# Performance work log

Measured on AMD Instinct MI355X. Metric: run time of the kernel, lower is better.

The kernel has to match this reference:

```python
import jax, jax.numpy as jnp
import numpy as np

EPS = 1e-5  # BatchNorm2d default eps


def conv1x1_bn(x, w, g, b, m, v):
    # 1x1 conv (no bias) + inference BatchNorm folded to scale/shift
    y = jnp.einsum('bchw,oc->bohw', x, w)
    s = g / jnp.sqrt(v + EPS)
    return y * s[None, :, None, None] + (b - m * s)[None, :, None, None]


def setup_inputs() -> dict:
    key = jax.random.key(0)
    ks = jax.random.split(key, 18)
    B, C, H, W = 4, 256, 64, 64
    KD, NH = 16, 8
    DH = KD * NH
    f = jax.random.normal
    u = jax.random.uniform
    return {
        'x': f(ks[0], (B, C, H, W), jnp.float32),
        'key_v_input_reduction': f(ks[1], (1,), jnp.float32),
        'w_qk': f(ks[2], (KD, C), jnp.float32) * 0.05,
        'g_qk': u(ks[3], (KD,), jnp.float32, 0.5, 1.5),
        'b_qk': f(ks[4], (KD,), jnp.float32) * 0.05,
        'm_qk': f(ks[5], (KD,), jnp.float32) * 0.05,
        'v_qk': u(ks[6], (KD,), jnp.float32, 0.5, 1.5),
        'w_v': f(ks[7], (DH, C), jnp.float32) * 0.05,
        'g_v': u(ks[8], (DH,), jnp.float32, 0.5, 1.5),
        'b_v': f(ks[9], (DH,), jnp.float32) * 0.05,
        'm_v': f(ks[10], (DH,), jnp.float32) * 0.05,
        'v_v': u(ks[11], (DH,), jnp.float32, 0.5, 1.5),
        'w_p': f(ks[12], (C, DH), jnp.float32) * 0.05,
        'g_p': u(ks[13], (C,), jnp.float32, 0.5, 1.5),
        'b_p': f(ks[14], (C,), jnp.float32) * 0.05,
        'm_p': f(ks[15], (C,), jnp.float32) * 0.05,
        'v_p': u(ks[16], (C,), jnp.float32, 0.5, 1.5),
    }


def reference(x, key_v_input_reduction, w_qk, g_qk, b_qk, m_qk, v_qk,
              w_v, g_v, b_v, m_v, v_v, w_p, g_p, b_p, m_p, v_p):
    B, C, H, W = x.shape
    N = H * W
    kd = w_qk.shape[0]
    dh = w_v.shape[0]
    nh = dh // kd
    # shared single KV head: qq == kk (share_kv=True, one_kv_head=True)
    qk = conv1x1_bn(x, w_qk, g_qk, b_qk, m_qk, v_qk).reshape(B, 1, kd, N)
    qq = jnp.swapaxes(qk, -1, -2)                      # [B,1,N,kd]
    attn = jax.nn.softmax(jnp.matmul(qq, qk), axis=-1)  # [B,1,N,N]
    vv = conv1x1_bn(x, w_v, g_v, b_v, m_v, v_v).reshape(B, nh, kd, N)
    vv = jnp.swapaxes(vv, -1, -2)                      # [B,nh,N,kd]
    xx = jnp.matmul(attn, vv)                          # broadcast head dim -> [B,nh,N,kd]
    xx = jnp.swapaxes(xx, -1, -2).reshape(B, dh, H, W)
    out = conv1x1_bn(jax.nn.relu(xx), w_p, g_p, b_p, m_p, v_p)
    return out
```

## Files before the change

### kernel.cpp

```cpp
#include <hip/hip_runtime.h>
#include <cstdint>
#include <cstddef>


typedef __attribute__((ext_vector_type(4)))  float f32x4;
typedef __attribute__((ext_vector_type(16))) float f32x16;
typedef __attribute__((ext_vector_type(8)))  _Float16 half8;
typedef __attribute__((ext_vector_type(8)))  unsigned short ushort8;
typedef __attribute__((ext_vector_type(2)))  unsigned u32x2;
typedef __attribute__((ext_vector_type(4)))  unsigned u32x4;

#define N_SP 4096
#define CIN  256
#define KDIM 16
#define DHV  128

__device__ __forceinline__ unsigned short f2h(float f) {
    _Float16 h = (_Float16)f;
    return __builtin_bit_cast(unsigned short, h);
}
__device__ __forceinline__ float h2f(unsigned short u) {
    return (float)__builtin_bit_cast(_Float16, u);
}
__device__ __forceinline__ unsigned pk2(float a, float b) {
    return (unsigned)f2h(a) | ((unsigned)f2h(b) << 16);
}
__device__ __forceinline__ unsigned shfl32u(unsigned v, int src) {
    return (unsigned)__shfl((int)v, src, 64);
}
__device__ __forceinline__ f32x4 mfma16(ushort8 a, ushort8 b, f32x4 c) {
    return __builtin_amdgcn_mfma_f32_16x16x32_f16(
        __builtin_bit_cast(half8, a), __builtin_bit_cast(half8, b), c, 0, 0, 0);
}
__device__ __forceinline__ f32x16 mfma32(half8 a, half8 b, f32x16 c) {
    return __builtin_amdgcn_mfma_f32_32x32x16_f16(a, b, c, 0, 0, 0);
}

__global__ __launch_bounds__(256) void fold_weights(
    const float* __restrict__ w_qk, const float* __restrict__ g_qk,
    const float* __restrict__ b_qk, const float* __restrict__ m_qk,
    const float* __restrict__ v_qk,
    const float* __restrict__ w_v, const float* __restrict__ g_v,
    const float* __restrict__ b_v, const float* __restrict__ m_v,
    const float* __restrict__ v_v,
    const float* __restrict__ w_p, const float* __restrict__ g_p,
    const float* __restrict__ b_p, const float* __restrict__ m_p,
    const float* __restrict__ v_p,
    unsigned short* __restrict__ wf1, float* __restrict__ shift1,
    unsigned short* __restrict__ wpf, float* __restrict__ shiftp)
{
    const float SQL2E = 1.2011224087864498f;
    int row = blockIdx.x;
    int t   = threadIdx.x;
    if (row < 144) {
        float s, sh; const float* src;
        if (row < KDIM) {
            s  = g_qk[row] * rsqrtf(v_qk[row] + 1e-5f);
            sh = b_qk[row] - m_qk[row] * s;
            s *= SQL2E; sh *= SQL2E;
            src = w_qk + row * CIN;
        } else {
            int o = row - KDIM;
            s  = g_v[o] * rsqrtf(v_v[o] + 1e-5f);
            sh = b_v[o] - m_v[o] * s;
            src = w_v + o * CIN;
        }
        wf1[row * CIN + t] = f2h(src[t] * s);
        if (t == 0) shift1[row] = sh;
    } else {
        int o = row - 144;
        float s = g_p[o] * rsqrtf(v_p[o] + 1e-5f);
        if (t < DHV) wpf[o * DHV + t] = f2h(w_p[o * DHV + t] * s);
        if (t == 0) shiftp[o] = b_p[o] - m_p[o] * s;
    }
}

__global__ __launch_bounds__(512) void proj_qkv(
    const float* __restrict__ x,
    const unsigned short* __restrict__ wf1, const float* __restrict__ shift1,
    unsigned short* __restrict__ qkT, unsigned short* __restrict__ Vt)
{
    const int b  = blockIdx.y;
    const int n0 = blockIdx.x * 64;
    const int tid  = threadIdx.x;
    const int w    = tid >> 6;
    const int half = w >> 2;
    const int wq   = w & 3;
    const int lane = tid & 63;
    const int lg   = lane >> 4;
    const int lr   = lane & 15;
    const int n    = n0 + wq * 16 + lr;

    const float* xb = x + (size_t)b * CIN * N_SP;

    if (half == 0) {
        f32x4 acc[5];
#pragma unroll
        for (int i = 0; i < 5; ++i) acc[i] = (f32x4){0.f, 0.f, 0.f, 0.f};
        for (int ks = 0; ks < 8; ++ks) {
            const int cbase = ks * 32 + lg * 8;
            ushort8 bx;
#pragma unroll
            for (int j = 0; j < 8; ++j)
                bx[j] = f2h(xb[(size_t)(cbase + j) * N_SP + n]);
#pragma unroll
            for (int i = 0; i < 5; ++i) {
                ushort8 a = *(const ushort8*)(wf1 + (i * 16 + lr) * CIN + cbase);
                acc[i] = mfma16(a, bx, acc[i]);
            }
        }
#pragma unroll
        for (int i = 0; i < 5; ++i)
#pragma unroll
            for (int r = 0; r < 4; ++r) {
                int o = i * 16 + lg * 4 + r;
                float val = acc[i][r] + shift1[o];
                unsigned short hv = f2h(val);
                if (o < KDIM) qkT[((size_t)b * N_SP + n) * 16 + o] = hv;
                else          Vt[((size_t)b * DHV + (o - KDIM)) * N_SP + n] = hv;
            }
    } else {
        f32x4 acc[4];
#pragma unroll
        for (int i = 0; i < 4; ++i) acc[i] = (f32x4){0.f, 0.f, 0.f, 0.f};
        for (int ks = 0; ks < 8; ++ks) {
            const int cbase = ks * 32 + lg * 8;
            ushort8 bx;
#pragma unroll
            for (int j = 0; j < 8; ++j)
                bx[j] = f2h(xb[(size_t)(cbase + j) * N_SP + n]);
#pragma unroll
            for (int i = 0; i < 4; ++i) {
                ushort8 a = *(const ushort8*)(wf1 + ((i + 5) * 16 + lr) * CIN + cbase);
                acc[i] = mfma16(a, bx, acc[i]);
            }
        }
#pragma unroll
        for (int i = 0; i < 4; ++i)
#pragma unroll
            for (int r = 0; r < 4; ++r) {
                int o = (i + 5) * 16 + lg * 4 + r;
                float val = acc[i][r] + shift1[o];
                Vt[((size_t)b * DHV + (o - KDIM)) * N_SP + n] = f2h(val);
            }
    }
}

__device__ __forceinline__ void stage_v(
    const unsigned short* __restrict__ vt_b,
    unsigned short* v_l, int k0, int p, int lane)
{
#pragma unroll
    for (int s = 0; s < 8; ++s) {
        const int vi = p * 8 + s;
        const int d  = vi * 8 + (lane >> 3);
        const int c8 = (lane & 7) ^ ((lane >> 3) & 7);
        const unsigned short* src = vt_b + (size_t)d * N_SP + k0 + c8 * 8;
        __builtin_amdgcn_global_load_lds(
            (const __attribute__((address_space(1))) void*)src,
            (__attribute__((address_space(3))) void*)(v_l + vi * 512),
            16, 0, 0);
    }
}

__device__ __forceinline__ half8 ldv(const unsigned short* vl, int nb, int kc,
                                     int la31, int hi)
{
    const int d = nb * 32 + la31;
    const ushort8 v = *(const ushort8*)
        (vl + d * 64 + (((kc * 2 + hi) ^ (d & 7)) << 3));
    return __builtin_bit_cast(half8, v);
}

__device__ __forceinline__ half8 ldk(const unsigned short* qk_b, int krow,
                                     int la31, int hi)
{
    return __builtin_bit_cast(half8,
        *(const ushort8*)(qk_b + (size_t)(krow + la31) * 16 + hi * 8));
}

__global__ __launch_bounds__(512, 2) void attn_kernel(
    const unsigned short* __restrict__ qkT,
    const unsigned short* __restrict__ Vt,
    const unsigned short* __restrict__ wpf,
    const float* __restrict__ shiftp,
    float* __restrict__ out)
{
    const int b  = blockIdx.y;
    const int q0 = blockIdx.x * 64;
    const int tid  = threadIdx.x;
    const int ws   = tid >> 6;
    const int strm = ws >> 1;
    const int p    = ws & 1;
    const int lane = tid & 63;
    const int la31 = lane & 31;
    const int hi   = lane >> 5;

    const unsigned short* qk_b = qkT + (size_t)b * N_SP * 16;
    const unsigned short* vt_b = Vt  + (size_t)b * DHV * N_SP;
    const int kbase = strm * (N_SP / 4);
    const int qrow  = q0 + p * 32;

    const half8 aq = __builtin_bit_cast(half8,
        *(const ushort8*)(qk_b + (size_t)(qrow + la31) * 16 + hi * 8));

    f32x16 acc0, acc1, acc2, acc3, z16;
#pragma unroll
    for (int i = 0; i < 16; ++i) { z16[i] = 0.f; }
    acc0 = z16; acc1 = z16; acc2 = z16; acc3 = z16;
    float m_r = -__builtin_inff();
    float l_r = 0.f;

    __shared__ __align__(16) unsigned short v_lds[4][2][128 * 64];
    __shared__ float lmbuf[4][64][2];

    stage_v(vt_b, &v_lds[strm][0][0], kbase, p, lane);
    half8 kf0n = ldk(qk_b, kbase, la31, hi);
    half8 kf1n = ldk(qk_b, kbase + 32, la31, hi);

    for (int t = 0; t < 16; ++t) {
        const int cur = t & 1;
        __syncthreads();
        if (t < 15)
            stage_v(vt_b, &v_lds[strm][cur ^ 1][0], kbase + (t + 1) * 64,
                    p, lane);
        const half8 kf0 = kf0n;
        const half8 kf1 = kf1n;
        if (t < 15) {
            kf0n = ldk(qk_b, kbase + (t + 1) * 64, la31, hi);
            kf1n = ldk(qk_b, kbase + (t + 1) * 64 + 32, la31, hi);
        }
        const unsigned short* vl = &v_lds[strm][cur][0];

        f32x16 s0 = mfma32(kf0, aq, z16);
        f32x16 s1 = mfma32(kf1, aq, z16);

        float mpair[8];
#pragma unroll
        for (int i = 0; i < 8; ++i)
            mpair[i] = fmaxf(fmaxf(s0[i], s0[i + 8]), fmaxf(s1[i], s1[i + 8]));
        float mx = fmaxf(fmaxf(fmaxf(mpair[0], mpair[1]), fmaxf(mpair[2], mpair[3])),
                         fmaxf(fmaxf(mpair[4], mpair[5]), fmaxf(mpair[6], mpair[7])));
        mx = fmaxf(mx, __shfl(mx, lane ^ 32));

        if (!__all(mx <= m_r + 11.54f)) {
            float mnew = fmaxf(m_r, mx);
            float sc = exp2f(m_r - mnew);
            l_r *= sc;
#pragma unroll
            for (int i = 0; i < 16; ++i) {
                acc0[i] *= sc; acc1[i] *= sc; acc2[i] *= sc; acc3[i] *= sc;
            }
            m_r = mnew;
        }
#pragma unroll
        for (int i = 0; i < 16; ++i) s0[i] = exp2f(s0[i] - m_r);
#pragma unroll
        for (int i = 0; i < 16; ++i) s1[i] = exp2f(s1[i] - m_r);
        float rpair[8];
#pragma unroll
        for (int i = 0; i < 8; ++i)
            rpair[i] = (s0[i] + s0[i + 8]) + (s1[i] + s1[i + 8]);
        l_r += ((rpair[0] + rpair[1]) + (rpair[2] + rpair[3]))
             + ((rpair[4] + rpair[5]) + (rpair[6] + rpair[7]));

#define PV_CHUNK(SV, B0, KC)                                               \
        {                                                                  \
            unsigned a0 = pk2(SV[B0 + 0], SV[B0 + 1]);                     \
            unsigned a1 = pk2(SV[B0 + 2], SV[B0 + 3]);                     \
            unsigned a2 = pk2(SV[B0 + 4], SV[B0 + 5]);                     \
            unsigned a3 = pk2(SV[B0 + 6], SV[B0 + 7]);                     \
            unsigned p0 = shfl32u(a0, lane ^ 32);                          \
            unsigned p1 = shfl32u(a1, lane ^ 32);                          \
            unsigned p2 = shfl32u(a2, lane ^ 32);                          \
            unsigned p3 = shfl32u(a3, lane ^ 32);                          \
            u32x4 pw;                                                      \
            pw.x = hi ? p2 : a0;                                           \
            pw.y = hi ? p3 : a1;                                           \
            pw.z = hi ? a2 : p0;                                           \
            pw.w = hi ? a3 : p1;                                           \
            half8 pb = __builtin_bit_cast(half8, pw);                      \
            acc0 = mfma32(ldv(vl, 0, KC, la31, hi), pb, acc0);             \
            acc1 = mfma32(ldv(vl, 1, KC, la31, hi), pb, acc1);             \
            acc2 = mfma32(ldv(vl, 2, KC, la31, hi), pb, acc2);             \
            acc3 = mfma32(ldv(vl, 3, KC, la31, hi), pb, acc3);             \
        }
        PV_CHUNK(s0, 0, 0)
        PV_CHUNK(s0, 8, 1)
        PV_CHUNK(s1, 0, 2)
        PV_CHUNK(s1, 8, 3)
#undef PV_CHUNK
    }

    l_r = l_r + __shfl(l_r, lane ^ 32);

    __syncthreads();

    unsigned short* Opart = &v_lds[0][0][0];
    const int qib = p * 32 + la31;
    if (hi == 0) {
        lmbuf[strm][qib][0] = m_r;
        lmbuf[strm][qib][1] = l_r;
    }
    {
        const float invl = 1.0f / l_r;
        const size_t qoff = ((size_t)strm * 64 + qib) * 128;
#define PUB(ACC, NB)                                                       \
        {                                                                  \
            _Pragma("unroll")                                              \
            for (int rq = 0; rq < 4; ++rq) {                               \
                float v0 = ACC[rq * 4 + 0] * invl;                         \
                float v1 = ACC[rq * 4 + 1] * invl;                         \
                float v2 = ACC[rq * 4 + 2] * invl;                         \
                float v3 = ACC[rq * 4 + 3] * invl;                         \
                u32x2 wv; wv.x = pk2(v0, v1); wv.y = pk2(v2, v3);          \
                *(u32x2*)(Opart + qoff + NB * 32 + rq * 8 + 4 * hi) = wv;  \
            }                                                              \
        }
        PUB(acc0, 0) PUB(acc1, 1) PUB(acc2, 2) PUB(acc3, 3)
#undef PUB
    }
    __syncthreads();

    unsigned short* olds = &v_lds[2][0][0];
    {
        const int q    = tid >> 3;
        const int dseg = (tid & 7) * 16;
        const float m0 = lmbuf[0][q][0], l0 = lmbuf[0][q][1];
        const float m1 = lmbuf[1][q][0], l1 = lmbuf[1][q][1];
        const float m2 = lmbuf[2][q][0], l2 = lmbuf[2][q][1];
        const float m3 = lmbuf[3][q][0], l3 = lmbuf[3][q][1];
        const float M = fmaxf(fmaxf(m0, m1), fmaxf(m2, m3));
        float w0 = l0 * exp2f(m0 - M);
        float w1 = l1 * exp2f(m1 - M);
        float w2 = l2 * exp2f(m2 - M);
        float w3 = l3 * exp2f(m3 - M);
        const float inv = 1.0f / (w0 + w1 + w2 + w3);
        w0 *= inv; w1 *= inv; w2 *= inv; w3 *= inv;

        const ushort8 A0 = *(const ushort8*)(Opart + (0 * 64 + q) * 128 + dseg);
        const ushort8 A1 = *(const ushort8*)(Opart + (1 * 64 + q) * 128 + dseg);
        const ushort8 A2 = *(const ushort8*)(Opart + (2 * 64 + q) * 128 + dseg);
        const ushort8 A3 = *(const ushort8*)(Opart + (3 * 64 + q) * 128 + dseg);
        const ushort8 B0 = *(const ushort8*)(Opart + (0 * 64 + q) * 128 + dseg + 8);
        const ushort8 B1 = *(const ushort8*)(Opart + (1 * 64 + q) * 128 + dseg + 8);
        const ushort8 B2 = *(const ushort8*)(Opart + (2 * 64 + q) * 128 + dseg + 8);
        const ushort8 B3 = *(const ushort8*)(Opart + (3 * 64 + q) * 128 + dseg + 8);

        ushort8 o0, o1;
#pragma unroll
        for (int i = 0; i < 8; ++i) {
            float va = w0 * h2f(A0[i]) + w1 * h2f(A1[i])
                     + w2 * h2f(A2[i]) + w3 * h2f(A3[i]);
            float vb = w0 * h2f(B0[i]) + w1 * h2f(B1[i])
                     + w2 * h2f(B2[i]) + w3 * h2f(B3[i]);
            o0[i] = f2h(fmaxf(va, 0.f));
            o1[i] = f2h(fmaxf(vb, 0.f));
        }
        *(ushort8*)(olds + q * 136 + dseg)     = o0;
        *(ushort8*)(olds + q * 136 + dseg + 8) = o1;
    }
    __syncthreads();

    {
        const int lr16 = lane & 15;
        const int lg16 = lane >> 4;
        const int ob   = ws * 32;

        f32x4 pacc[2][4];
#pragma unroll
        for (int i = 0; i < 2; ++i)
#pragma unroll
            for (int j = 0; j < 4; ++j) pacc[i][j] = (f32x4){0.f, 0.f, 0.f, 0.f};

        for (int ks = 0; ks < 4; ++ks) {
            ushort8 a0 = *(const ushort8*)
                (wpf + (size_t)(ob + lr16) * DHV + ks * 32 + lg16 * 8);
            ushort8 a1 = *(const ushort8*)
                (wpf + (size_t)(ob + 16 + lr16) * DHV + ks * 32 + lg16 * 8);
#pragma unroll
            for (int qt = 0; qt < 4; ++qt) {
                ushort8 bfr = *(const ushort8*)
                    (olds + (qt * 16 + lr16) * 136 + ks * 32 + lg16 * 8);
                pacc[0][qt] = mfma16(a0, bfr, pacc[0][qt]);
                pacc[1][qt] = mfma16(a1, bfr, pacc[1][qt]);
            }
        }

#pragma unroll
        for (int t2 = 0; t2 < 2; ++t2)
#pragma unroll
            for (int qt = 0; qt < 4; ++qt)
#pragma unroll
                for (int r = 0; r < 4; ++r) {
                    int o = ob + t2 * 16 + lg16 * 4 + r;
                    out[((size_t)b * CIN + o) * N_SP + q0 + qt * 16 + lr16]
                        = pacc[t2][qt][r] + shiftp[o];
                }
    }
}

extern "C" void kernel_launch(void* const* d_in, const int* in_sizes, int n_in,
                              void* d_out, int out_size, void* d_ws, size_t ws_size,
                              hipStream_t stream)
{
    const float* x    = (const float*)d_in[0];
    const float* w_qk = (const float*)d_in[2];
    const float* g_qk = (const float*)d_in[3];
    const float* b_qk = (const float*)d_in[4];
    const float* m_qk = (const float*)d_in[5];
    const float* v_qk = (const float*)d_in[6];
    const float* w_v  = (const float*)d_in[7];
    const float* g_v  = (const float*)d_in[8];
    const float* b_v  = (const float*)d_in[9];
    const float* m_v  = (const float*)d_in[10];
    const float* v_v  = (const float*)d_in[11];
    const float* w_p  = (const float*)d_in[12];
    const float* g_p  = (const float*)d_in[13];
    const float* b_p  = (const float*)d_in[14];
    const float* m_p  = (const float*)d_in[15];
    const float* v_p  = (const float*)d_in[16];

    char* ws = (char*)d_ws;
    unsigned short* qkT = (unsigned short*)(ws);
    unsigned short* Vt  = (unsigned short*)(ws + (1u << 20));
    unsigned short* wf1 = (unsigned short*)(ws + (9u << 20));
    float* shift1       = (float*)(ws + (9u << 20) + 80 * 1024);
    unsigned short* wpf = (unsigned short*)(ws + (9u << 20) + 84 * 1024);
    float* shiftp       = (float*)(ws + (9u << 20) + 148 * 1024);

    fold_weights<<<400, 256, 0, stream>>>(
        w_qk, g_qk, b_qk, m_qk, v_qk,
        w_v, g_v, b_v, m_v, v_v,
        w_p, g_p, b_p, m_p, v_p,
        wf1, shift1, wpf, shiftp);

    proj_qkv<<<dim3(64, 4), 512, 0, stream>>>(x, wf1, shift1, qkT, Vt);

    attn_kernel<<<dim3(64, 4), 512, 0, stream>>>(
        qkT, Vt, wpf, shiftp, (float*)d_out);
}
```

Before: 69.94 us.

## Split attention keys across eight wave-pair streams with 1024-thread blocks

The attention kernel now runs 1024 threads per block, so the key dimension is split into 8 streams instead of 4. Each stream handles 512 keys in 32-key tiles with a narrower swizzled LDS V buffer, and the final merge combines 8 partial outputs. The projection epilogue gives each wave 16 output channels instead of 32. The aim is more waves per CU to hide latency in the key loop. The cost is a larger cross-stream merge, more barriers per tile, and heavier register pressure under the new launch bounds.

```diff
diff --git a/kernel.cpp b/kernel.cpp
--- a/kernel.cpp
+++ b/kernel.cpp
@@ -151,11 +151,12 @@
     unsigned short* v_l, int k0, int p, int lane)
 {
 #pragma unroll
-    for (int s = 0; s < 8; ++s) {
-        const int vi = p * 8 + s;
-        const int d  = vi * 8 + (lane >> 3);
-        const int c8 = (lane & 7) ^ ((lane >> 3) & 7);
-        const unsigned short* src = vt_b + (size_t)d * N_SP + k0 + c8 * 8;
+    for (int s = 0; s < 4; ++s) {
+        const int vi   = p * 4 + s;
+        const int dloc = lane >> 2;
+        const int d    = vi * 16 + dloc;
+        const int c4   = (lane & 3) ^ (dloc & 3);
+        const unsigned short* src = vt_b + (size_t)d * N_SP + k0 + c4 * 8;
         __builtin_amdgcn_global_load_lds(
             (const __attribute__((address_space(1))) void*)src,
             (__attribute__((address_space(3))) void*)(v_l + vi * 512),
@@ -168,7 +169,7 @@
 {
     const int d = nb * 32 + la31;
     const ushort8 v = *(const ushort8*)
-        (vl + d * 64 + (((kc * 2 + hi) ^ (d & 7)) << 3));
+        (vl + d * 32 + (((kc * 2 + hi) ^ (d & 3)) << 3));
     return __builtin_bit_cast(half8, v);
 }
 
@@ -179,7 +180,7 @@
         *(const ushort8*)(qk_b + (size_t)(krow + la31) * 16 + hi * 8));
 }
 
-__global__ __launch_bounds__(512, 2) void attn_kernel(
+__global__ __launch_bounds__(1024, 4) void attn_kernel(
     const unsigned short* __restrict__ qkT,
     const unsigned short* __restrict__ Vt,
     const unsigned short* __restrict__ wpf,
@@ -198,7 +199,7 @@
 
     const unsigned short* qk_b = qkT + (size_t)b * N_SP * 16;
     const unsigned short* vt_b = Vt  + (size_t)b * DHV * N_SP;
-    const int kbase = strm * (N_SP / 4);
+    const int kbase = strm * (N_SP / 8);
     const int qrow  = q0 + p * 32;
 
     const half8 aq = __builtin_bit_cast(half8,
@@ -211,34 +212,28 @@
     float m_r = -__builtin_inff();
     float l_r = 0.f;
 
-    __shared__ __align__(16) unsigned short v_lds[4][2][128 * 64];
-    __shared__ float lmbuf[4][64][2];
+    __shared__ __align__(16) unsigned short v_lds[8][2][128 * 32];
+    __shared__ float lmbuf[8][64][2];
 
     stage_v(vt_b, &v_lds[strm][0][0], kbase, p, lane);
     half8 kf0n = ldk(qk_b, kbase, la31, hi);
-    half8 kf1n = ldk(qk_b, kbase + 32, la31, hi);
 
     for (int t = 0; t < 16; ++t) {
         const int cur = t & 1;
         __syncthreads();
         if (t < 15)
-            stage_v(vt_b, &v_lds[strm][cur ^ 1][0], kbase + (t + 1) * 64,
+            stage_v(vt_b, &v_lds[strm][cur ^ 1][0], kbase + (t + 1) * 32,
                     p, lane);
         const half8 kf0 = kf0n;
-        const half8 kf1 = kf1n;
-        if (t < 15) {
-            kf0n = ldk(qk_b, kbase + (t + 1) * 64, la31, hi);
-            kf1n = ldk(qk_b, kbase + (t + 1) * 64 + 32, la31, hi);
-        }
+        if (t < 15)
+            kf0n = ldk(qk_b, kbase + (t + 1) * 32, la31, hi);
         const unsigned short* vl = &v_lds[strm][cur][0];
 
         f32x16 s0 = mfma32(kf0, aq, z16);
-        f32x16 s1 = mfma32(kf1, aq, z16);
 
         float mpair[8];
 #pragma unroll
-        for (int i = 0; i < 8; ++i)
-            mpair[i] = fmaxf(fmaxf(s0[i], s0[i + 8]), fmaxf(s1[i], s1[i + 8]));
+        for (int i = 0; i < 8; ++i) mpair[i] = fmaxf(s0[i], s0[i + 8]);
         float mx = fmaxf(fmaxf(fmaxf(mpair[0], mpair[1]), fmaxf(mpair[2], mpair[3])),
                          fmaxf(fmaxf(mpair[4], mpair[5]), fmaxf(mpair[6], mpair[7])));
         mx = fmaxf(mx, __shfl(mx, lane ^ 32));
@@ -255,12 +250,9 @@
         }
 #pragma unroll
         for (int i = 0; i < 16; ++i) s0[i] = exp2f(s0[i] - m_r);
-#pragma unroll
-        for (int i = 0; i < 16; ++i) s1[i] = exp2f(s1[i] - m_r);
         float rpair[8];
 #pragma unroll
-        for (int i = 0; i < 8; ++i)
-            rpair[i] = (s0[i] + s0[i + 8]) + (s1[i] + s1[i + 8]);
+        for (int i = 0; i < 8; ++i) rpair[i] = s0[i] + s0[i + 8];
         l_r += ((rpair[0] + rpair[1]) + (rpair[2] + rpair[3]))
              + ((rpair[4] + rpair[5]) + (rpair[6] + rpair[7]));
 
@@ -287,8 +279,6 @@
         }
         PV_CHUNK(s0, 0, 0)
         PV_CHUNK(s0, 8, 1)
-        PV_CHUNK(s1, 0, 2)
-        PV_CHUNK(s1, 8, 3)
 #undef PV_CHUNK
     }
 
@@ -322,81 +312,66 @@
     }
     __syncthreads();
 
-    unsigned short* olds = &v_lds[2][0][0];
+    unsigned short* olds = &v_lds[0][0][0];
     {
-        const int q    = tid >> 3;
-        const int dseg = (tid & 7) * 16;
-        const float m0 = lmbuf[0][q][0], l0 = lmbuf[0][q][1];
-        const float m1 = lmbuf[1][q][0], l1 = lmbuf[1][q][1];
-        const float m2 = lmbuf[2][q][0], l2 = lmbuf[2][q][1];
-        const float m3 = lmbuf[3][q][0], l3 = lmbuf[3][q][1];
-        const float M = fmaxf(fmaxf(m0, m1), fmaxf(m2, m3));
-        float w0 = l0 * exp2f(m0 - M);
-        float w1 = l1 * exp2f(m1 - M);
-        float w2 = l2 * exp2f(m2 - M);
-        float w3 = l3 * exp2f(m3 - M);
-        const float inv = 1.0f / (w0 + w1 + w2 + w3);
-        w0 *= inv; w1 *= inv; w2 *= inv; w3 *= inv;
-
-        const ushort8 A0 = *(const ushort8*)(Opart + (0 * 64 + q) * 128 + dseg);
-        const ushort8 A1 = *(const ushort8*)(Opart + (1 * 64 + q) * 128 + dseg);
-        const ushort8 A2 = *(const ushort8*)(Opart + (2 * 64 + q) * 128 + dseg);
-        const ushort8 A3 = *(const ushort8*)(Opart + (3 * 64 + q) * 128 + dseg);
-        const ushort8 B0 = *(const ushort8*)(Opart + (0 * 64 + q) * 128 + dseg + 8);
-        const ushort8 B1 = *(const ushort8*)(Opart + (1 * 64 + q) * 128 + dseg + 8);
-        const ushort8 B2 = *(const ushort8*)(Opart + (2 * 64 + q) * 128 + dseg + 8);
-        const ushort8 B3 = *(const ushort8*)(Opart + (3 * 64 + q) * 128 + dseg + 8);
-
-        ushort8 o0, o1;
+        const int q    = tid >> 4;
+        const int dseg = (tid & 15) * 8;
+
+        ushort8 part[8];
+        float   wgt[8];
+        float M = -__builtin_inff();
+#pragma unroll
+        for (int s = 0; s < 8; ++s) M = fmaxf(M, lmbuf[s][q][0]);
+        float wsum = 0.f;
+#pragma unroll
+        for (int s = 0; s < 8; ++s) {
+            wgt[s] = lmbuf[s][q][1] * exp2f(lmbuf[s][q][0] - M);
+            wsum += wgt[s];
+            part[s] = *(const ushort8*)(Opart + ((size_t)s * 64 + q) * 128 + dseg);
+        }
+        const float inv = 1.0f / wsum;
+
+        ushort8 o8;
 #pragma unroll
         for (int i = 0; i < 8; ++i) {
-            float va = w0 * h2f(A0[i]) + w1 * h2f(A1[i])
-                     + w2 * h2f(A2[i]) + w3 * h2f(A3[i]);
-            float vb = w0 * h2f(B0[i]) + w1 * h2f(B1[i])
-                     + w2 * h2f(B2[i]) + w3 * h2f(B3[i]);
-            o0[i] = f2h(fmaxf(va, 0.f));
-            o1[i] = f2h(fmaxf(vb, 0.f));
-        }
-        *(ushort8*)(olds + q * 136 + dseg)     = o0;
-        *(ushort8*)(olds + q * 136 + dseg + 8) = o1;
+            float v = 0.f;
+#pragma unroll
+            for (int s = 0; s < 8; ++s) v += wgt[s] * h2f(part[s][i]);
+            o8[i] = f2h(fmaxf(v * inv, 0.f));
+        }
+        __syncthreads();
+        *(ushort8*)(olds + q * 136 + dseg) = o8;
     }
     __syncthreads();
 
     {
         const int lr16 = lane & 15;
         const int lg16 = lane >> 4;
-        const int ob   = ws * 32;
-
-        f32x4 pacc[2][4];
-#pragma unroll
-        for (int i = 0; i < 2; ++i)
-#pragma unroll
-            for (int j = 0; j < 4; ++j) pacc[i][j] = (f32x4){0.f, 0.f, 0.f, 0.f};
+        const int ob   = ws * 16;
+
+        f32x4 pacc[4];
+#pragma unroll
+        for (int i = 0; i < 4; ++i) pacc[i] = (f32x4){0.f, 0.f, 0.f, 0.f};
 
         for (int ks = 0; ks < 4; ++ks) {
-            ushort8 a0 = *(const ushort8*)
+            ushort8 a = *(const ushort8*)
                 (wpf + (size_t)(ob + lr16) * DHV + ks * 32 + lg16 * 8);
-            ushort8 a1 = *(const ushort8*)
-                (wpf + (size_t)(ob + 16 + lr16) * DHV + ks * 32 + lg16 * 8);
 #pragma unroll
             for (int qt = 0; qt < 4; ++qt) {
                 ushort8 bfr = *(const ushort8*)
                     (olds + (qt * 16 + lr16) * 136 + ks * 32 + lg16 * 8);
-                pacc[0][qt] = mfma16(a0, bfr, pacc[0][qt]);
-                pacc[1][qt] = mfma16(a1, bfr, pacc[1][qt]);
-            }
-        }
-
-#pragma unroll
-        for (int t2 = 0; t2 < 2; ++t2)
-#pragma unroll
-            for (int qt = 0; qt < 4; ++qt)
-#pragma unroll
-                for (int r = 0; r < 4; ++r) {
-                    int o = ob + t2 * 16 + lg16 * 4 + r;
-                    out[((size_t)b * CIN + o) * N_SP + q0 + qt * 16 + lr16]
-                        = pacc[t2][qt][r] + shiftp[o];
-                }
+                pacc[qt] = mfma16(a, bfr, pacc[qt]);
+            }
+        }
+
+#pragma unroll
+        for (int qt = 0; qt < 4; ++qt)
+#pragma unroll
+            for (int r = 0; r < 4; ++r) {
+                int o = ob + lg16 * 4 + r;
+                out[((size_t)b * CIN + o) * N_SP + q0 + qt * 16 + lr16]
+                    = pacc[qt][r] + shiftp[o];
+            }
     }
 }
 
@@ -437,6 +412,6 @@
 
     proj_qkv<<<dim3(64, 4), 512, 0, stream>>>(x, wf1, shift1, qkT, Vt);
 
-    attn_kernel<<<dim3(64, 4), 512, 0, stream>>>(
+    attn_kernel<<<dim3(64, 4), 1024, 0, stream>>>(
         qkT, Vt, wpf, shiftp, (float*)d_out);
 }
```

Measured after the change: 76.77 us. 9.8% more time.
